# Kernel tuning notes

Measured on AMD Instinct MI355X. Metric: run time of the kernel, lower is better.

## Reference

```python
import jax, jax.numpy as jnp
import numpy as np

N_BINS = 15


def setup_inputs() -> dict:
    key = jax.random.key(0)
    k1, k2 = jax.random.split(key)
    B, C = 524288, 128
    logits = jax.random.normal(k1, (B, C), dtype=jnp.float32)
    labels = jax.random.randint(k2, (B,), 0, C)
    return {"logits": logits, "labels": labels}


def reference(logits, labels):
    n_bins = N_BINS
    B, C = logits.shape
    probs = jax.nn.softmax(logits, axis=1)                      # [B, C]
    onehot = jax.nn.one_hot(labels, C, dtype=probs.dtype)       # [B, C]

    # bin b holds conf in (boundaries[b], boundaries[b+1]]
    boundaries = jnp.linspace(0.0, 1.0, n_bins + 1)
    idx = jnp.searchsorted(boundaries, probs, side="left") - 1  # [B, C]
    idx = jnp.clip(idx, 0, n_bins - 1)
    valid = probs > 0.0  # conf == 0 falls in no bin (strict lower bound)

    # fused (class, bin) segment id; invalid elements go to a trash segment
    seg = jnp.where(valid, idx + jnp.arange(C)[None, :] * n_bins, C * n_bins)
    flat_seg = seg.reshape(-1)
    num_seg = C * n_bins + 1

    conf_sum = jax.ops.segment_sum(probs.reshape(-1), flat_seg, num_segments=num_seg)[:-1]
    acc_sum = jax.ops.segment_sum(onehot.reshape(-1), flat_seg, num_segments=num_seg)[:-1]
    counts = jax.ops.segment_sum(jnp.ones((B * C,), probs.dtype), flat_seg, num_segments=num_seg)[:-1]

    safe = jnp.maximum(counts, 1.0)
    gap = jnp.abs(conf_sum / safe - acc_sum / safe)             # |avg_conf - avg_acc| per (class,bin)
    sce = jnp.sum(jnp.where(counts > 0, gap * counts / B, 0.0)) / C
    return sce.reshape(1)
```

## Files before the change

### kernel.cpp

```cpp
#include <hip/hip_runtime.h>
#include <cmath>

#define NBINS 15
#define NCLS  128
#define NSEG  (NCLS * NBINS)
#define BLK   512
#define GRID  1024
#define NWAVES (GRID * (BLK / 64))

__global__ __launch_bounds__(BLK, 8) void sce_hist_kernel(
    const float* __restrict__ logits, const int* __restrict__ labels,
    float* __restrict__ pconf, float* __restrict__ pacc, int B)
{
    __shared__ float s_conf[NSEG];
    __shared__ float s_acc[NSEG];
    for (int i = threadIdx.x; i < NSEG; i += BLK) { s_conf[i] = 0.f; s_acc[i] = 0.f; }
    __syncthreads();

    const int lane  = threadIdx.x & 63;
    const int wave  = threadIdx.x >> 6;
    const int sub   = lane >> 4;
    const int q     = lane & 15;
    const int cbase = q * 4;
    const float db  = 1.0f / 15.0f;

    float conf0[8];
#pragma unroll
    for (int j = 0; j < 8; ++j) conf0[j] = 0.f;

    const int wgid = blockIdx.x * (BLK / 64) + wave;
    const int G = (B + 3) >> 2;

    for (int g0 = wgid; g0 < G; g0 += 2 * NWAVES) {
        float4 v0[2], v1[2];
        int lab[2]; bool val[2];
#pragma unroll
        for (int u = 0; u < 2; ++u) {
            int g = g0 + u * NWAVES;
            int row = 4 * g + sub;
            val[u] = (g < G) && (row < B);
            int r = val[u] ? row : 0;
            const float4* rp = (const float4*)(logits + (size_t)r * NCLS);
            v0[u] = rp[q];
            v1[u] = rp[q + 16];
            lab[u] = labels[r];
        }
        float e[2][8], s[2];
#pragma unroll
        for (int u = 0; u < 2; ++u) {
            e[u][0] = __expf(v0[u].x); e[u][1] = __expf(v0[u].y);
            e[u][2] = __expf(v0[u].z); e[u][3] = __expf(v0[u].w);
            e[u][4] = __expf(v1[u].x); e[u][5] = __expf(v1[u].y);
            e[u][6] = __expf(v1[u].z); e[u][7] = __expf(v1[u].w);
            s[u] = ((e[u][0] + e[u][1]) + (e[u][2] + e[u][3]))
                 + ((e[u][4] + e[u][5]) + (e[u][6] + e[u][7]));
        }
#pragma unroll
        for (int off = 1; off <= 8; off <<= 1) {
#pragma unroll
            for (int u = 0; u < 2; ++u) s[u] += __shfl_xor(s[u], off);
        }
#pragma unroll
        for (int u = 0; u < 2; ++u) {
            float inv = 1.0f / s[u];
#pragma unroll
            for (int j = 0; j < 8; ++j) {
                int c = (j < 4) ? (cbase + j) : (64 + cbase + j - 4);
                float p = e[u][j] * inv;
                bool fast = (p <= db);
                conf0[j] += (val[u] && fast) ? p : 0.f;
                if (val[u] && (!fast || c == lab[u])) {
                    int b = (int)(p * 15.0f);
                    b = b > 14 ? 14 : b;
                    b += (p > (float)(b + 1) * db) ? 1 : 0;
                    b -= (p <= (float)b * db) ? 1 : 0;
                    if (!fast) atomicAdd(&s_conf[c * NBINS + b], p);
                    if (c == lab[u]) atomicAdd(&s_acc[lab[u] * NBINS + b], 1.0f);
                }
            }
        }
    }

#pragma unroll
    for (int j = 0; j < 8; ++j) {
        int c = (j < 4) ? (cbase + j) : (64 + cbase + j - 4);
        atomicAdd(&s_conf[c * NBINS], conf0[j]);
    }
    __syncthreads();

    float* pc = pconf + (size_t)blockIdx.x * NSEG;
    float* pa = pacc  + (size_t)blockIdx.x * NSEG;
    for (int i = threadIdx.x; i < NSEG; i += BLK) {
        pc[i] = s_conf[i];
        pa[i] = s_acc[i];
    }
}

__global__ __launch_bounds__(256) void sce_reduce_kernel(
    const float* __restrict__ pconf, const float* __restrict__ pacc,
    float* __restrict__ out, float scale)
{
    __shared__ float s_d[256];
    const int seg = blockIdx.x * 32 + (threadIdx.x & 31);
    const int p0  = threadIdx.x >> 5;
    float d = 0.f;
#pragma unroll 8
    for (int p = p0; p < GRID; p += 8) {
        d += pconf[(size_t)p * NSEG + seg] - pacc[(size_t)p * NSEG + seg];
    }
    s_d[threadIdx.x] = d;
    __syncthreads();
    if (threadIdx.x < 32) {
        float t = 0.f;
#pragma unroll
        for (int j = 0; j < 8; ++j) t += s_d[threadIdx.x + 32 * j];
        t = fabsf(t);
#pragma unroll
        for (int off = 16; off; off >>= 1) t += __shfl_xor(t, off);
        if (threadIdx.x == 0) atomicAdd(out, t * scale);
    }
}

extern "C" void kernel_launch(void* const* d_in, const int* in_sizes, int n_in,
                              void* d_out, int out_size, void* d_ws, size_t ws_size,
                              hipStream_t stream)
{
    const float* logits = (const float*)d_in[0];
    const int*   labels = (const int*)d_in[1];
    float* out = (float*)d_out;
    int B = in_sizes[1];

    float* pconf = (float*)d_ws;
    float* pacc  = pconf + (size_t)GRID * NSEG;

    hipMemsetAsync(d_out, 0, sizeof(float), stream);

    sce_hist_kernel<<<GRID, BLK, 0, stream>>>(logits, labels, pconf, pacc, B);

    const float scale = 1.0f / ((float)B * (float)NCLS);
    sce_reduce_kernel<<<NSEG / 32, 256, 0, stream>>>(pconf, pacc, out, scale);
}
```

Baseline: 384.4 us.

## Software-pipeline logit loads and split label-accuracy atomics from the confidence path

Restructures the histogram loop into a full-tile main loop that prefetches the next pair of row groups into registers while computing the current one, plus a separate tail loop for leftover rows. It removes per-element validity checks in the main loop and moves the label accuracy atomic out of the per-class loop, so only the one lane holding the label does it. It also swaps the division for a hardware reciprocal and lowers the launch-bounds occupancy hint from 8 to 4 blocks per CU. The prefetch buffers add register pressure and may reduce occupancy, and the reciprocal is approximate, which could move borderline probabilities into a different bin.

```diff
diff --git a/kernel.cpp b/kernel.cpp
--- a/kernel.cpp
+++ b/kernel.cpp
@@ -6,9 +6,18 @@
 #define NSEG  (NCLS * NBINS)
 #define BLK   512
 #define GRID  1024
-#define NWAVES (GRID * (BLK / 64))
-
-__global__ __launch_bounds__(BLK, 8) void sce_hist_kernel(
+#define WPB   (BLK / 64)
+#define NWAVES (GRID * WPB)
+
+__device__ __forceinline__ int bin_of(float p, float db) {
+    int b = (int)(p * 15.0f);
+    b = b > 14 ? 14 : b;
+    b += (p > (float)(b + 1) * db) ? 1 : 0;
+    b -= (p <= (float)b * db) ? 1 : 0;
+    return b;
+}
+
+__global__ __launch_bounds__(BLK, 4) void sce_hist_kernel(
     const float* __restrict__ logits, const int* __restrict__ labels,
     float* __restrict__ pconf, float* __restrict__ pacc, int B)
 {
@@ -28,23 +37,39 @@
 #pragma unroll
     for (int j = 0; j < 8; ++j) conf0[j] = 0.f;
 
-    const int wgid = blockIdx.x * (BLK / 64) + wave;
-    const int G = (B + 3) >> 2;
-
-    for (int g0 = wgid; g0 < G; g0 += 2 * NWAVES) {
-        float4 v0[2], v1[2];
-        int lab[2]; bool val[2];
+    const int wgid  = blockIdx.x * WPB + wave;
+    const int Gfull = B >> 2;
+    const int nfull = Gfull / (2 * NWAVES);
+
+    float4 nv0[2], nv1[2]; int nlab[2];
+    int gbase = wgid;
+    if (nfull > 0) {
 #pragma unroll
         for (int u = 0; u < 2; ++u) {
-            int g = g0 + u * NWAVES;
-            int row = 4 * g + sub;
-            val[u] = (g < G) && (row < B);
-            int r = val[u] ? row : 0;
-            const float4* rp = (const float4*)(logits + (size_t)r * NCLS);
-            v0[u] = rp[q];
-            v1[u] = rp[q + 16];
-            lab[u] = labels[r];
-        }
+            int row = 4 * (gbase + u * NWAVES) + sub;
+            const float4* rp = (const float4*)(logits + (size_t)row * NCLS);
+            nv0[u] = rp[q];
+            nv1[u] = rp[q + 16];
+            nlab[u] = labels[row];
+        }
+    }
+
+    for (int it = 0; it < nfull; ++it) {
+        float4 v0[2], v1[2]; int lab[2];
+#pragma unroll
+        for (int u = 0; u < 2; ++u) { v0[u] = nv0[u]; v1[u] = nv1[u]; lab[u] = nlab[u]; }
+        gbase += 2 * NWAVES;
+        if (it + 1 < nfull) {
+#pragma unroll
+            for (int u = 0; u < 2; ++u) {
+                int row = 4 * (gbase + u * NWAVES) + sub;
+                const float4* rp = (const float4*)(logits + (size_t)row * NCLS);
+                nv0[u] = rp[q];
+                nv1[u] = rp[q + 16];
+                nlab[u] = labels[row];
+            }
+        }
+
         float e[2][8], s[2];
 #pragma unroll
         for (int u = 0; u < 2; ++u) {
@@ -62,20 +87,55 @@
         }
 #pragma unroll
         for (int u = 0; u < 2; ++u) {
-            float inv = 1.0f / s[u];
+            float inv = __builtin_amdgcn_rcpf(s[u]);
+            int lb = lab[u];
+            if (q == ((lb & 63) >> 2)) {
+                int j = (lb & 3) + ((lb >= 64) ? 4 : 0);
+                float p = e[u][j] * inv;
+                atomicAdd(&s_acc[lb * NBINS + bin_of(p, db)], 1.0f);
+            }
 #pragma unroll
             for (int j = 0; j < 8; ++j) {
-                int c = (j < 4) ? (cbase + j) : (64 + cbase + j - 4);
                 float p = e[u][j] * inv;
                 bool fast = (p <= db);
-                conf0[j] += (val[u] && fast) ? p : 0.f;
-                if (val[u] && (!fast || c == lab[u])) {
-                    int b = (int)(p * 15.0f);
-                    b = b > 14 ? 14 : b;
-                    b += (p > (float)(b + 1) * db) ? 1 : 0;
-                    b -= (p <= (float)b * db) ? 1 : 0;
-                    if (!fast) atomicAdd(&s_conf[c * NBINS + b], p);
-                    if (c == lab[u]) atomicAdd(&s_acc[lab[u] * NBINS + b], 1.0f);
+                conf0[j] += fast ? p : 0.f;
+                if (!fast) {
+                    int c = (j < 4) ? (cbase + j) : (64 + cbase + j - 4);
+                    atomicAdd(&s_conf[c * NBINS + bin_of(p, db)], p);
+                }
+            }
+        }
+    }
+
+    const int Gall = (B + 3) >> 2;
+    for (int g = nfull * 2 * NWAVES + wgid; g < Gall; g += NWAVES) {
+        int row = 4 * g + sub;
+        bool val = row < B;
+        int r = val ? row : 0;
+        const float4* rp = (const float4*)(logits + (size_t)r * NCLS);
+        float4 v0 = rp[q], v1 = rp[q + 16];
+        int lb = labels[r];
+        float e[8];
+        e[0] = __expf(v0.x); e[1] = __expf(v0.y); e[2] = __expf(v0.z); e[3] = __expf(v0.w);
+        e[4] = __expf(v1.x); e[5] = __expf(v1.y); e[6] = __expf(v1.z); e[7] = __expf(v1.w);
+        float s = ((e[0] + e[1]) + (e[2] + e[3])) + ((e[4] + e[5]) + (e[6] + e[7]));
+#pragma unroll
+        for (int off = 1; off <= 8; off <<= 1) s += __shfl_xor(s, off);
+        float inv = __builtin_amdgcn_rcpf(s);
+        if (val) {
+            if (q == ((lb & 63) >> 2)) {
+                int j = (lb & 3) + ((lb >= 64) ? 4 : 0);
+                float p = e[j] * inv;
+                atomicAdd(&s_acc[lb * NBINS + bin_of(p, db)], 1.0f);
+            }
+#pragma unroll
+            for (int j = 0; j < 8; ++j) {
+                float p = e[j] * inv;
+                bool fast = (p <= db);
+                conf0[j] += fast ? p : 0.f;
+                if (!fast) {
+                    int c = (j < 4) ? (cbase + j) : (64 + cbase + j - 4);
+                    atomicAdd(&s_conf[c * NBINS + bin_of(p, db)], p);
                 }
             }
         }
```

Result: slower. 423.4 us (+10.2%).
